# Performance work log

Measured on AMD Instinct MI355X. Metric: run time of the kernel, lower is better.

## Reference

```python
import jax, jax.numpy as jnp
import numpy as np

N = 50000   # nodes
E = 500000  # edges (before self-loops)
D = 256     # out_dim
H = 8       # heads
HD = D // H # head dim
NEG = 0.2   # leaky relu slope (both GAT attention and module act)


def setup_inputs() -> dict:
    key = jax.random.key(0)
    ks = jax.random.split(key, 16)
    s = 0.05
    feats = jax.random.normal(ks[0], (N, D), jnp.float32)
    src = jax.random.randint(ks[1], (E,), 0, N, jnp.int32)
    dst = jax.random.randint(ks[2], (E,), 0, N, jnp.int32)
    proj_W = jax.random.normal(ks[3], (D, D), jnp.float32) * s
    proj_b = jnp.zeros((D,), jnp.float32)
    W1 = jax.random.normal(ks[4], (D, D), jnp.float32) * s
    al1 = jax.random.normal(ks[5], (H, HD), jnp.float32) * s
    ar1 = jax.random.normal(ks[6], (H, HD), jnp.float32) * s
    b1 = jnp.zeros((D,), jnp.float32)
    W2 = jax.random.normal(ks[7], (D, D), jnp.float32) * s
    al2 = jax.random.normal(ks[8], (H, HD), jnp.float32) * s
    ar2 = jax.random.normal(ks[9], (H, HD), jnp.float32) * s
    b2 = jnp.zeros((D,), jnp.float32)
    return dict(feats=feats, src=src, dst=dst, proj_W=proj_W, proj_b=proj_b,
                W1=W1, al1=al1, ar1=ar1, b1=b1, W2=W2, al2=al2, ar2=ar2, b2=b2)


def gat_layer(x, W, al, ar, b, src, dst):
    # x: [N, D] -> h: [N, H, HD]
    h = (x @ W).reshape(N, H, HD)
    el = jnp.einsum('nhd,hd->nh', h, al)   # [N, H]
    er = jnp.einsum('nhd,hd->nh', h, ar)
    e = jax.nn.leaky_relu(el[src] + er[dst], NEG)  # [E+N, H]
    # edge softmax over destination neighborhoods
    m = jax.ops.segment_max(e, dst, num_segments=N)       # [N, H]
    a = jnp.exp(e - m[dst])
    z = jax.ops.segment_sum(a, dst, num_segments=N)       # [N, H]
    alpha = a / z[dst]                                     # [E+N, H]
    out = jax.ops.segment_sum(alpha[:, :, None] * h[src], dst, num_segments=N)  # [N,H,HD]
    out = out + b.reshape(H, HD)
    return out.reshape(N, D)


def reference(feats, src, dst, proj_W, proj_b, W1, al1, ar1, b1, W2, al2, ar2, b2):
    # dgl.add_self_loop
    loop = jnp.arange(N, dtype=src.dtype)
    s = jnp.concatenate([src, loop])
    d = jnp.concatenate([dst, loop])
    x = feats @ proj_W + proj_b
    for W, al, ar, b in ((W1, al1, ar1, b1), (W2, al2, ar2, b2)):
        x = gat_layer(x, W, al, ar, b, s, d)
        x = jax.nn.leaky_relu(x, NEG)  # module act; dropout = eval no-op
    return x
```

## Files before the change

### kernel.cpp

```cpp
#include <hip/hip_runtime.h>
#include <stdint.h>
#include <stddef.h>

#define NNODES 50000
#define NEDGES 500000
#define DIM 256
#define NHEAD 8
#define HDIM 32
#define MPAD 50048
#define NEGS 0.2f
#define SCAN_BLOCKS 196
#define COUNT_BLOCKS 1954
#define CVT_BLOCKS 12500
#define TR_BLOCKS 192
#define GEMM_BLOCKS 782

typedef __attribute__((ext_vector_type(8))) short bf16x8;
typedef __attribute__((ext_vector_type(4))) float f32x4;
typedef __attribute__((ext_vector_type(4))) unsigned short u16x4;

__device__ __forceinline__ unsigned short f2bf(float f) {
    uint32_t u = __builtin_bit_cast(uint32_t, f);
    uint32_t r = (u + 0x7FFFu + ((u >> 16) & 1u)) >> 16;
    return (unsigned short)r;
}

__device__ __forceinline__ float bf2f(unsigned short u) {
    return __builtin_bit_cast(float, (uint32_t)u << 16);
}

__device__ __forceinline__ float bf2f_s(short u) {
    return __builtin_bit_cast(float, (uint32_t)(unsigned short)u << 16);
}

__device__ __forceinline__ float leaky(float x) {
    return x > 0.0f ? x : NEGS * x;
}

__device__ __forceinline__ void gld_lds16(const unsigned short* g, unsigned short* l) {
    __builtin_amdgcn_global_load_lds(
        (const __attribute__((address_space(1))) void*)g,
        (__attribute__((address_space(3))) void*)l,
        16, 0, 0);
}

__device__ __forceinline__ void xcd_pair(int orig, int& bx, int& by) {
    int x = orig & 7, g = orig >> 3;
    int v = (x < 6 ? x * 98 : 588 + (x - 6) * 97) + g;
    bx = v >> 1;
    by = v & 1;
}


__global__ __launch_bounds__(256) void scanA_kernel(const int* __restrict__ deg,
                                                    int* __restrict__ bsum) {
    __shared__ int ws[4];
    int t = threadIdx.x;
    int idx = blockIdx.x * 256 + t;
    int v = (idx < NNODES) ? deg[idx] : 0;
    int x = v;
    #pragma unroll
    for (int off = 1; off < 64; off <<= 1) x += __shfl_xor(x, off, 64);
    if ((t & 63) == 0) ws[t >> 6] = x;
    __syncthreads();
    if (t == 0) bsum[blockIdx.x] = ws[0] + ws[1] + ws[2] + ws[3];
}

__global__ __launch_bounds__(256) void scanB_kernel(const int* __restrict__ bsum,
                                                    int* __restrict__ boff,
                                                    int* __restrict__ rowptr) {
    __shared__ int s[256];
    int t = threadIdx.x;
    int v = (t < SCAN_BLOCKS) ? bsum[t] : 0;
    s[t] = v;
    __syncthreads();
    #pragma unroll
    for (int off = 1; off < 256; off <<= 1) {
        int y = (t >= off) ? s[t - off] : 0;
        __syncthreads();
        s[t] += y;
        __syncthreads();
    }
    if (t < SCAN_BLOCKS) boff[t] = s[t] - v;
    if (t == 0) rowptr[NNODES] = NEDGES;
}

__global__ __launch_bounds__(256) void scanC_kernel(const int* __restrict__ deg,
                                                    const int* __restrict__ boff,
                                                    int* __restrict__ rowptr,
                                                    int* __restrict__ cursor) {
    __shared__ int ws[4];
    int t = threadIdx.x;
    int lane = t & 63, wv = t >> 6;
    int idx = blockIdx.x * 256 + t;
    int v = (idx < NNODES) ? deg[idx] : 0;
    int x = v;
    #pragma unroll
    for (int off = 1; off < 64; off <<= 1) {
        int y = __shfl_up(x, off, 64);
        if (lane >= off) x += y;
    }
    if (lane == 63) ws[wv] = x;
    __syncthreads();
    int wadd = 0;
    #pragma unroll
    for (int k = 0; k < 4; ++k) if (k < wv) wadd += ws[k];
    int excl = x - v + wadd + boff[blockIdx.x];
    if (idx < NNODES) { rowptr[idx] = excl; cursor[idx] = excl; }
}


__global__ __launch_bounds__(256) void combo1(const int* __restrict__ dst,
                                              int* __restrict__ deg,
                                              const float* __restrict__ feats,
                                              unsigned short* __restrict__ Abf,
                                              const float* __restrict__ W0,
                                              const float* __restrict__ W1,
                                              const float* __restrict__ W2,
                                              unsigned short* __restrict__ WT) {
    __shared__ float tile[32][33];
    int b = blockIdx.x;
    if (b < COUNT_BLOCKS) {
        int i = b * 256 + threadIdx.x;
        if (i < NEDGES) atomicAdd(&deg[dst[i]], 1);
    } else if (b < COUNT_BLOCKS + CVT_BLOCKS) {
        int i = ((b - COUNT_BLOCKS) * 256 + threadIdx.x) * 4;
        const float4 v = *(const float4*)(feats + i);
        u16x4 o;
        o.x = f2bf(v.x); o.y = f2bf(v.y); o.z = f2bf(v.z); o.w = f2bf(v.w);
        *(u16x4*)(Abf + i) = o;
    } else {
        int t = b - COUNT_BLOCKS - CVT_BLOCKS;
        int bz = t >> 6;
        int bx = t & 7;
        int by = (t >> 3) & 7;
        const float* W = (bz == 0) ? W0 : (bz == 1) ? W1 : W2;
        unsigned short* T = WT + (size_t)bz * DIM * DIM;
        int tx = threadIdx.x & 31, ty = threadIdx.x >> 5;
        #pragma unroll
        for (int j = 0; j < 4; ++j)
            tile[ty + j * 8][tx] = W[(by * 32 + ty + j * 8) * DIM + bx * 32 + tx];
        __syncthreads();
        #pragma unroll
        for (int j = 0; j < 4; ++j)
            T[(bx * 32 + ty + j * 8) * DIM + by * 32 + tx] = f2bf(tile[tx][ty + j * 8]);
    }
}


__device__ __forceinline__ void gemm_body(int bx, int by,
        const unsigned short* __restrict__ A, const unsigned short* __restrict__ BT,
        unsigned short* __restrict__ Cb, const float* __restrict__ bias) {
    __shared__ __align__(16) unsigned short As[2][128][32];
    __shared__ __align__(16) unsigned short Bs[2][128][32];
    int tid = threadIdx.x;
    int wave = tid >> 6, lane = tid & 63;
    int row0 = bx * 128;
    int col0 = by * 128;
    int wm = (wave >> 1) * 64;
    int wn = (wave & 1) * 64;

    f32x4 acc[4][4] = {};

    int fr = lane & 15;
    int kg = (lane >> 4) * 8;

    #pragma unroll
    for (int kt = 0; kt < 4; ++kt) {
        #pragma unroll
        for (int r = 0; r < 4; ++r) {
            int idx = r * 256 + tid;
            int c = idx >> 9;
            int rem = idx & 511;
            int row = rem >> 2;
            int q = rem & 3;
            gld_lds16(A + (size_t)(row0 + row) * DIM + kt * 64 + c * 32 + q * 8,
                      &As[0][0][0] + idx * 8);
            gld_lds16(BT + (size_t)(col0 + row) * DIM + kt * 64 + c * 32 + q * 8,
                      &Bs[0][0][0] + idx * 8);
        }
        __syncthreads();

        #pragma unroll
        for (int c = 0; c < 2; ++c) {
            bf16x8 a_frag[4], b_frag[4];
            #pragma unroll
            for (int i = 0; i < 4; ++i) {
                a_frag[i] = *(const bf16x8*)(&As[c][wm + i * 16 + fr][kg]);
                b_frag[i] = *(const bf16x8*)(&Bs[c][wn + i * 16 + fr][kg]);
            }
            #pragma unroll
            for (int i = 0; i < 4; ++i)
                #pragma unroll
                for (int j = 0; j < 4; ++j)
                    acc[i][j] = __builtin_amdgcn_mfma_f32_16x16x32_bf16(
                        a_frag[i], b_frag[j], acc[i][j], 0, 0, 0);
        }
        __syncthreads();
    }

    int rg = (lane >> 4) * 4;
    #pragma unroll
    for (int i = 0; i < 4; ++i) {
        #pragma unroll
        for (int j = 0; j < 4; ++j) {
            int n = col0 + wn + j * 16 + fr;
            float bv = bias ? bias[n] : 0.0f;
            #pragma unroll
            for (int r = 0; r < 4; ++r) {
                int m = row0 + wm + i * 16 + rg + r;
                Cb[(size_t)m * DIM + n] = f2bf(acc[i][j][r] + bv);
            }
        }
    }
}

__global__ __launch_bounds__(256, 4) void gemm_kernel(const unsigned short* __restrict__ A,
                                                      const unsigned short* __restrict__ BT,
                                                      unsigned short* __restrict__ Cb,
                                                      const float* __restrict__ bias) {
    int bx, by;
    xcd_pair(blockIdx.x, bx, by);
    gemm_body(bx, by, A, BT, Cb, bias);
}


__global__ __launch_bounds__(256, 4) void combo2(const unsigned short* __restrict__ A,
                                                 const unsigned short* __restrict__ BT,
                                                 unsigned short* __restrict__ Cb,
                                                 const float* __restrict__ bias,
                                                 const int* __restrict__ src,
                                                 const int* __restrict__ dst,
                                                 int* __restrict__ cursor,
                                                 int* __restrict__ csr) {
    int b = blockIdx.x;
    if (b < GEMM_BLOCKS) {
        int bx, by;
        xcd_pair(b, bx, by);
        gemm_body(bx, by, A, BT, Cb, bias);
    } else {
        int i = (b - GEMM_BLOCKS) * 256 + threadIdx.x;
        if (i < NEDGES) {
            int pos = atomicAdd(&cursor[dst[i]], 1);
            csr[pos] = src[i];
        }
    }
}


__global__ __launch_bounds__(256) void agg_kernel(const unsigned short* __restrict__ Hb,
                                                  const float* __restrict__ al,
                                                  const float* __restrict__ ar,
                                                  const int* __restrict__ rowptr,
                                                  const int* __restrict__ csr,
                                                  const float* __restrict__ bias,
                                                  float* __restrict__ outf,
                                                  unsigned short* __restrict__ outb) {
    int wave = threadIdx.x >> 6;
    int lane = threadIdx.x & 63;
    int v = blockIdx.x * 4 + wave;
    if (v >= NNODES) return;
    int sub = lane & 31;
    int halfe = lane >> 5;
    int c0 = sub * 8;

    float4 a0 = *(const float4*)(al + c0);
    float4 a1 = *(const float4*)(al + c0 + 4);
    float4 g0 = *(const float4*)(ar + c0);
    float4 g1 = *(const float4*)(ar + c0 + 4);

    bf16x8 hv = *(const bf16x8*)(Hb + (size_t)v * DIM + c0);
    float hvf[8];
    #pragma unroll
    for (int d = 0; d < 8; ++d) hvf[d] = bf2f_s(hv[d]);
    float dl = hvf[0] * a0.x + hvf[1] * a0.y + hvf[2] * a0.z + hvf[3] * a0.w
             + hvf[4] * a1.x + hvf[5] * a1.y + hvf[6] * a1.z + hvf[7] * a1.w;
    float dr = hvf[0] * g0.x + hvf[1] * g0.y + hvf[2] * g0.z + hvf[3] * g0.w
             + hvf[4] * g1.x + hvf[5] * g1.y + hvf[6] * g1.z + hvf[7] * g1.w;
    dl += __shfl_xor(dl, 1, 64); dl += __shfl_xor(dl, 2, 64);
    dr += __shfl_xor(dr, 1, 64); dr += __shfl_xor(dr, 2, 64);
    float el_v = dl, er_v = dr;

    int beg = rowptr[v], end = rowptr[v + 1];

    float z = 0.0f;
    float acc[8] = {0.f, 0.f, 0.f, 0.f, 0.f, 0.f, 0.f, 0.f};

    if (halfe == 0) {
        float ws = __expf(leaky(el_v + er_v));
        z = ws;
        #pragma unroll
        for (int d = 0; d < 8; ++d) acc[d] = ws * hvf[d];
    }

    #pragma unroll 4
    for (int i = beg + halfe; i < end; i += 2) {
        int u = csr[i];
        bf16x8 h = *(const bf16x8*)(Hb + (size_t)u * DIM + c0);
        float hf[8];
        #pragma unroll
        for (int d = 0; d < 8; ++d) hf[d] = bf2f_s(h[d]);
        float du = hf[0] * a0.x + hf[1] * a0.y + hf[2] * a0.z + hf[3] * a0.w
                 + hf[4] * a1.x + hf[5] * a1.y + hf[6] * a1.z + hf[7] * a1.w;
        du += __shfl_xor(du, 1, 64);
        du += __shfl_xor(du, 2, 64);
        float e = leaky(du + er_v);
        float wi = __expf(e);
        z += wi;
        #pragma unroll
        for (int d = 0; d < 8; ++d) acc[d] += wi * hf[d];
    }

    z += __shfl_xor(z, 32, 64);
    #pragma unroll
    for (int d = 0; d < 8; ++d) acc[d] += __shfl_xor(acc[d], 32, 64);

    float inv = 1.0f / z;
    int o0 = c0 + halfe * 4;
    float4 b = *(const float4*)(bias + o0);
    float r0 = leaky(acc[halfe * 4 + 0] * inv + b.x);
    float r1 = leaky(acc[halfe * 4 + 1] * inv + b.y);
    float r2 = leaky(acc[halfe * 4 + 2] * inv + b.z);
    float r3 = leaky(acc[halfe * 4 + 3] * inv + b.w);
    if (outf) {
        float4 o = { r0, r1, r2, r3 };
        *(float4*)(outf + (size_t)v * DIM + o0) = o;
    } else {
        u16x4 o;
        o.x = f2bf(r0); o.y = f2bf(r1); o.z = f2bf(r2); o.w = f2bf(r3);
        *(u16x4*)(outb + (size_t)v * DIM + o0) = o;
    }
}


static inline size_t align256(size_t x) { return (x + 255) & ~(size_t)255; }

extern "C" void kernel_launch(void* const* d_in, const int* in_sizes, int n_in,
                              void* d_out, int out_size, void* d_ws, size_t ws_size,
                              hipStream_t stream) {
    const float* feats  = (const float*)d_in[0];
    const int*   src    = (const int*)d_in[1];
    const int*   dst    = (const int*)d_in[2];
    const float* proj_W = (const float*)d_in[3];
    const float* proj_b = (const float*)d_in[4];
    const float* W1     = (const float*)d_in[5];
    const float* al1    = (const float*)d_in[6];
    const float* ar1    = (const float*)d_in[7];
    const float* b1     = (const float*)d_in[8];
    const float* W2     = (const float*)d_in[9];
    const float* al2    = (const float*)d_in[10];
    const float* ar2    = (const float*)d_in[11];
    const float* b2     = (const float*)d_in[12];
    float* out = (float*)d_out;

    uint8_t* w = (uint8_t*)d_ws;
    unsigned short* Abf = (unsigned short*)w; w += align256((size_t)MPAD * DIM * 2);
    unsigned short* Bbf = (unsigned short*)w; w += align256((size_t)MPAD * DIM * 2);
    unsigned short* Hb  = (unsigned short*)w; w += align256((size_t)MPAD * DIM * 2);
    unsigned short* WT  = (unsigned short*)w; w += align256((size_t)3 * DIM * DIM * 2);
    int* deg    = (int*)w;            w += align256((size_t)NNODES * 4);
    int* rowptr = (int*)w;            w += align256((size_t)(NNODES + 1) * 4);
    int* cursor = (int*)w;            w += align256((size_t)NNODES * 4);
    int* csr    = (int*)w;            w += align256((size_t)NEDGES * 4);
    int* bsum   = (int*)w;            w += align256((size_t)SCAN_BLOCKS * 4);
    int* boff   = (int*)w;            w += align256((size_t)SCAN_BLOCKS * 4);

    unsigned short* WT0 = WT;
    unsigned short* WT1 = WT + (size_t)DIM * DIM;
    unsigned short* WT2 = WT + (size_t)2 * DIM * DIM;

    const int node_wave_blocks = (NNODES + 3) / 4;

    hipMemsetAsync(deg, 0, (size_t)NNODES * 4, stream);

    combo1<<<COUNT_BLOCKS + CVT_BLOCKS + TR_BLOCKS, 256, 0, stream>>>(
        dst, deg, feats, Abf, proj_W, W1, W2, WT);

    scanA_kernel<<<SCAN_BLOCKS, 256, 0, stream>>>(deg, bsum);
    scanB_kernel<<<1, 256, 0, stream>>>(bsum, boff, rowptr);
    scanC_kernel<<<SCAN_BLOCKS, 256, 0, stream>>>(deg, boff, rowptr, cursor);

    combo2<<<GEMM_BLOCKS + COUNT_BLOCKS, 256, 0, stream>>>(
        Abf, WT0, Bbf, proj_b, src, dst, cursor, csr);

    gemm_kernel<<<GEMM_BLOCKS, 256, 0, stream>>>(Bbf, WT1, Hb, nullptr);
    agg_kernel<<<node_wave_blocks, 256, 0, stream>>>(Hb, al1, ar1, rowptr, csr, b1,
                                                     nullptr, Abf);

    gemm_kernel<<<GEMM_BLOCKS, 256, 0, stream>>>(Abf, WT2, Hb, nullptr);
    agg_kernel<<<node_wave_blocks, 256, 0, stream>>>(Hb, al2, ar2, rowptr, csr, b2,
                                                     out, nullptr);
}
```

Baseline: 310.8 us.

## Double-buffer GEMM LDS tiles with 32-wide K stages to overlap loads and MFMA

The GEMM main loop now loads 32-wide K slices into alternating LDS buffers. The next slice is prefetched while MFMAs run on the current one, so the loop needs one barrier per stage instead of two per 64-wide chunk. The aim is to hide global-to-LDS load latency behind compute. It doubles the number of K iterations, and correctness depends on the async LDS loads having finished before the single barrier.

```diff
diff --git a/kernel.cpp b/kernel.cpp
--- a/kernel.cpp
+++ b/kernel.cpp
@@ -165,39 +165,42 @@
     int fr = lane & 15;
     int kg = (lane >> 4) * 8;
 
-    #pragma unroll
-    for (int kt = 0; kt < 4; ++kt) {
-        #pragma unroll
-        for (int r = 0; r < 4; ++r) {
-            int idx = r * 256 + tid;
-            int c = idx >> 9;
-            int rem = idx & 511;
-            int row = rem >> 2;
-            int q = rem & 3;
-            gld_lds16(A + (size_t)(row0 + row) * DIM + kt * 64 + c * 32 + q * 8,
-                      &As[0][0][0] + idx * 8);
-            gld_lds16(BT + (size_t)(col0 + row) * DIM + kt * 64 + c * 32 + q * 8,
-                      &Bs[0][0][0] + idx * 8);
+    #define STAGE32(buf, kt)                                                      \
+        do {                                                                      \
+            _Pragma("unroll")                                                     \
+            for (int r_ = 0; r_ < 2; ++r_) {                                      \
+                int idx_ = r_ * 256 + tid;                                        \
+                int row_ = idx_ >> 2;                                             \
+                int q_ = idx_ & 3;                                                \
+                gld_lds16(A + (size_t)(row0 + row_) * DIM + (kt) * 32 + q_ * 8,   \
+                          &As[buf][0][0] + idx_ * 8);                             \
+                gld_lds16(BT + (size_t)(col0 + row_) * DIM + (kt) * 32 + q_ * 8,  \
+                          &Bs[buf][0][0] + idx_ * 8);                             \
+            }                                                                     \
+        } while (0)
+
+    STAGE32(0, 0);
+    __syncthreads();
+
+    int cur = 0;
+    #pragma unroll
+    for (int kt = 0; kt < 8; ++kt) {
+        if (kt < 7) STAGE32(cur ^ 1, kt + 1);
+        bf16x8 a_frag[4], b_frag[4];
+        #pragma unroll
+        for (int i = 0; i < 4; ++i) {
+            a_frag[i] = *(const bf16x8*)(&As[cur][wm + i * 16 + fr][kg]);
+            b_frag[i] = *(const bf16x8*)(&Bs[cur][wn + i * 16 + fr][kg]);
         }
-        __syncthreads();
-
-        #pragma unroll
-        for (int c = 0; c < 2; ++c) {
-            bf16x8 a_frag[4], b_frag[4];
+        #pragma unroll
+        for (int i = 0; i < 4; ++i)
             #pragma unroll
-            for (int i = 0; i < 4; ++i) {
-                a_frag[i] = *(const bf16x8*)(&As[c][wm + i * 16 + fr][kg]);
-                b_frag[i] = *(const bf16x8*)(&Bs[c][wn + i * 16 + fr][kg]);
-            }
-            #pragma unroll
-            for (int i = 0; i < 4; ++i)
-                #pragma unroll
-                for (int j = 0; j < 4; ++j)
-                    acc[i][j] = __builtin_amdgcn_mfma_f32_16x16x32_bf16(
-                        a_frag[i], b_frag[j], acc[i][j], 0, 0, 0);
-        }
-        __syncthreads();
-    }
+            for (int j = 0; j < 4; ++j)
+                acc[i][j] = __builtin_amdgcn_mfma_f32_16x16x32_bf16(
+                    a_frag[i], b_frag[j], acc[i][j], 0, 0, 0);
+        if (kt < 7) { __syncthreads(); cur ^= 1; }
+    }
+    #undef STAGE32
 
     int rg = (lane >> 4) * 4;
     #pragma unroll
```

Result: no change. 306.7 us (-1.3%).
